# Kernel tuning notes

Measured on AMD Instinct MI355X. Metric: run time of the kernel, lower is better.

## Reference

```python
import jax, jax.numpy as jnp
import numpy as np
import math

D_MODEL = 1024
NUM_HEADS = 16
NUM_LAYERS = 4
D_FF = 4096
TEXT_DIM = 512
B, SV, ST = 4, 2048, 100
EPS = 1e-5


def positional_encoding(seq_len, d):
    pos = jnp.arange(seq_len, dtype=jnp.float32)[:, None]
    div = jnp.exp(jnp.arange(0, d, 2, dtype=jnp.float32) * (-math.log(10000.0) / d))
    pe = jnp.zeros((seq_len, d), dtype=jnp.float32)
    pe = pe.at[:, 0::2].set(jnp.sin(pos * div))
    pe = pe.at[:, 1::2].set(jnp.cos(pos * div))
    return pe  # [seq_len, d]


def layer_norm(x, g, b):
    mu = jnp.mean(x, axis=-1, keepdims=True)
    var = jnp.mean(jnp.square(x - mu), axis=-1, keepdims=True)
    return (x - mu) * jax.lax.rsqrt(var + EPS) * g + b


def setup_inputs() -> dict:
    key = jax.random.key(0)
    ks = jax.random.split(key, 24)
    s = 0.02
    inp = {
        "video": jax.random.normal(ks[0], (B, SV, D_MODEL), jnp.float32),
        "text": jax.random.normal(ks[1], (B, ST, TEXT_DIM), jnp.float32),
        "text_mask": jnp.ones((B, ST), jnp.int32),
        # stacked per-layer params, weights stored [in, out]
        "Wq_w": jax.random.normal(ks[2], (NUM_LAYERS, D_MODEL, D_MODEL)) * s,
        "Wq_b": jnp.zeros((NUM_LAYERS, D_MODEL)),
        "Wk_w": jax.random.normal(ks[3], (NUM_LAYERS, TEXT_DIM, D_MODEL)) * s,
        "Wk_b": jnp.zeros((NUM_LAYERS, D_MODEL)),
        "Wv_w": jax.random.normal(ks[4], (NUM_LAYERS, TEXT_DIM, D_MODEL)) * s,
        "Wv_b": jnp.zeros((NUM_LAYERS, D_MODEL)),
        "Wo_w": jax.random.normal(ks[5], (NUM_LAYERS, D_MODEL, D_MODEL)) * s,
        "Wo_b": jnp.zeros((NUM_LAYERS, D_MODEL)),
        "fc1_w": jax.random.normal(ks[6], (NUM_LAYERS, D_MODEL, D_FF)) * s,
        "fc1_b": jnp.zeros((NUM_LAYERS, D_FF)),
        "fc2_w": jax.random.normal(ks[7], (NUM_LAYERS, D_FF, D_MODEL)) * s,
        "fc2_b": jnp.zeros((NUM_LAYERS, D_MODEL)),
        "n2_g": jnp.ones((NUM_LAYERS, D_MODEL)),
        "n2_b": jnp.zeros((NUM_LAYERS, D_MODEL)),
        "n3_g": jnp.ones((NUM_LAYERS, D_MODEL)),
        "n3_b": jnp.zeros((NUM_LAYERS, D_MODEL)),
    }
    return inp


def cross_attn_layer(video, text, mask, wq, bq, wk, bk, wv, bv, wo, bo):
    Bv, Sq, D = video.shape
    H, dk = NUM_HEADS, D_MODEL // NUM_HEADS
    q = (video @ wq + bq).reshape(Bv, Sq, H, dk).transpose(0, 2, 1, 3)  # bhqd
    k = (text @ wk + bk).reshape(Bv, -1, H, dk).transpose(0, 2, 1, 3)   # bhkd
    v = (text @ wv + bv).reshape(Bv, -1, H, dk).transpose(0, 2, 1, 3)
    scores = jnp.einsum("bhqd,bhkd->bhqk", q, k) / math.sqrt(dk)
    scores = jnp.where(mask, scores, jnp.float32(-1e9))
    probs = jax.nn.softmax(scores, axis=-1)
    out = jnp.einsum("bhqk,bhkd->bhqd", probs, v)
    out = out.transpose(0, 2, 1, 3).reshape(Bv, Sq, D)
    return out @ wo + bo


def reference(video, text, text_mask, Wq_w, Wq_b, Wk_w, Wk_b, Wv_w, Wv_b,
              Wo_w, Wo_b, fc1_w, fc1_b, fc2_w, fc2_b, n2_g, n2_b, n3_g, n3_b):
    video = video + positional_encoding(SV, D_MODEL)[None, :video.shape[1]]
    text = text + positional_encoding(ST, TEXT_DIM)[None, :text.shape[1]]
    mask = (text_mask != 0)[:, None, None, :]  # [B,1,1,St]
    for l in range(NUM_LAYERS):
        attn = cross_attn_layer(video, text, mask,
                                Wq_w[l], Wq_b[l], Wk_w[l], Wk_b[l],
                                Wv_w[l], Wv_b[l], Wo_w[l], Wo_b[l])
        video = layer_norm(video + attn, n2_g[l], n2_b[l])
        ff = jax.nn.relu(video @ fc1_w[l] + fc1_b[l]) @ fc2_w[l] + fc2_b[l]
        video = layer_norm(video + ff, n3_g[l], n3_b[l])
    return video
```

## Files before the change

kernel.cpp:

```cpp
#include <hip/hip_runtime.h>
#include <cstdint>
#include <cstddef>

typedef unsigned short u16;
typedef __attribute__((ext_vector_type(8))) __bf16 bf16x8;
typedef __attribute__((ext_vector_type(4))) float f32x4;

__device__ __forceinline__ f32x4 mfma_16x16x32(bf16x8 a, bf16x8 b, f32x4 c) {
  return __builtin_amdgcn_mfma_f32_16x16x32_bf16(a, b, c, 0, 0, 0);
}

__device__ __forceinline__ u16 f2bf(float f) {
  union { float f; uint32_t u; } c; c.f = f;
  uint32_t u = c.u + 0x7FFFu + ((c.u >> 16) & 1u);
  return (u16)(u >> 16);
}

__device__ __forceinline__ float bf2f(u16 x) {
  union { uint32_t u; float f; } c; c.u = ((uint32_t)x) << 16;
  return c.f;
}

__device__ __forceinline__ void gload_lds16(const void* g, void* l) {
  __builtin_amdgcn_global_load_lds(
      (__attribute__((address_space(1))) void*)(uintptr_t)g,
      (__attribute__((address_space(3))) void*)l, 16, 0, 0);
}

template<int MR, bool OUT_BF16, bool RELU, bool ACC>
__global__ __launch_bounds__(512, 2) void gemm_ring(
    const u16* __restrict__ A, int lda, const u16* __restrict__ Bt, int ldb,
    const float* __restrict__ bias, void* Cout, int ldc,
    int M, int N, int K)
{
  constexpr int BM = MR * 32;
  constexpr int SLOT = (BM + 256) * 32;
  __shared__ u16 ring[4 * SLOT];

  const int tid = threadIdx.x;
  const int lane = tid & 63, wave = tid >> 6;
  const int wm = wave >> 2, wn = wave & 3;
  const int m0 = blockIdx.x * BM, n0 = blockIdx.y * 256;

  const int cA0 = tid;
  const int rA0 = cA0 >> 2;
  const u16* gA0 = A + (size_t)(m0 + rA0) * lda + (((cA0 & 3) ^ (rA0 & 3)) * 8);
  const int cA1 = tid + 512;
  const int rA1 = cA1 >> 2;
  const u16* gA1 = A + (size_t)(m0 + (MR == 8 ? rA1 : 0)) * lda + (((cA1 & 3) ^ (rA1 & 3)) * 8);
  const int cB0 = tid, cB1 = tid + 512;
  const int rB0 = cB0 >> 2, rB1 = cB1 >> 2;
  const u16* gB0 = Bt + (size_t)(n0 + rB0) * ldb + (((cB0 & 3) ^ (rB0 & 3)) * 8);
  const u16* gB1 = Bt + (size_t)(n0 + rB1) * ldb + (((cB1 & 3) ^ (rB1 & 3)) * 8);

  const int NK = K >> 5;

  auto STAGE = [&](int s) {
    u16* Sb = &ring[(s & 3) * SLOT];
    const int ko = s * 32;
    gload_lds16(gA0 + ko, Sb + cA0 * 8);
    if constexpr (MR == 8) gload_lds16(gA1 + ko, Sb + cA1 * 8);
    gload_lds16(gB0 + ko, Sb + BM * 32 + cB0 * 8);
    gload_lds16(gB1 + ko, Sb + BM * 32 + cB1 * 8);
  };
  auto WAITV = [&](int ahead) {
    if (ahead >= 2) {
      if constexpr (MR == 8) asm volatile("s_waitcnt vmcnt(8)" ::: "memory");
      else                   asm volatile("s_waitcnt vmcnt(6)" ::: "memory");
    } else if (ahead == 1) {
      if constexpr (MR == 8) asm volatile("s_waitcnt vmcnt(4)" ::: "memory");
      else                   asm volatile("s_waitcnt vmcnt(3)" ::: "memory");
    } else {
      asm volatile("s_waitcnt vmcnt(0)" ::: "memory");
    }
    __builtin_amdgcn_sched_barrier(0);
  };

  const int fr = lane & 15, g = lane >> 4;
  const int sw = g ^ (fr & 3);
  const int foff = fr * 32 + sw * 8;

  f32x4 acc[MR][4];
  #pragma unroll
  for (int m = 0; m < MR; m++)
    #pragma unroll
    for (int n = 0; n < 4; n++) acc[m][n] = f32x4{0.f, 0.f, 0.f, 0.f};

  for (int i = 0; i < 3; ++i) if (i < NK) STAGE(i);
  {
    int im = (NK - 1 < 2) ? NK - 1 : 2;
    WAITV(im);
  }
  __builtin_amdgcn_s_barrier();
  __builtin_amdgcn_sched_barrier(0);

  for (int s = 0; s < NK; ++s) {
    const u16* Sb = &ring[(s & 3) * SLOT];
    const u16* As = Sb;
    const u16* Bs = Sb + BM * 32;

    bf16x8 bf[4];
    #pragma unroll
    for (int n = 0; n < 4; n++)
      bf[n] = *(const bf16x8*)(Bs + (wn * 64 + n * 16) * 32 + foff);
    {
      bf16x8 af[MR / 2];
      #pragma unroll
      for (int m = 0; m < MR / 2; m++)
        af[m] = *(const bf16x8*)(As + (wm * (MR * 16) + m * 16) * 32 + foff);
      if (s + 3 < NK) STAGE(s + 3);
      __builtin_amdgcn_s_barrier();
      asm volatile("s_waitcnt lgkmcnt(0)" ::: "memory");
      __builtin_amdgcn_sched_barrier(0);
      __builtin_amdgcn_s_setprio(1);
      #pragma unroll
      for (int m = 0; m < MR / 2; m++)
        #pragma unroll
        for (int n = 0; n < 4; n++)
          acc[m][n] = mfma_16x16x32(af[m], bf[n], acc[m][n]);
      __builtin_amdgcn_s_setprio(0);
      __builtin_amdgcn_s_barrier();
      __builtin_amdgcn_sched_barrier(0);
    }
    {
      bf16x8 af[MR / 2];
      #pragma unroll
      for (int m = 0; m < MR / 2; m++)
        af[m] = *(const bf16x8*)(As + (wm * (MR * 16) + (m + MR / 2) * 16) * 32 + foff);
      __builtin_amdgcn_s_barrier();
      asm volatile("s_waitcnt lgkmcnt(0)" ::: "memory");
      __builtin_amdgcn_sched_barrier(0);
      __builtin_amdgcn_s_setprio(1);
      #pragma unroll
      for (int m = 0; m < MR / 2; m++)
        #pragma unroll
        for (int n = 0; n < 4; n++)
          acc[m + MR / 2][n] = mfma_16x16x32(af[m], bf[n], acc[m + MR / 2][n]);
      __builtin_amdgcn_s_setprio(0);
      {
        int im = (s + 3 < NK - 1) ? s + 3 : NK - 1;
        WAITV(im - (s + 1));
      }
      __builtin_amdgcn_s_barrier();
      __builtin_amdgcn_sched_barrier(0);
    }
  }

  #pragma unroll
  for (int n = 0; n < 4; n++) {
    const int gcol = n0 + wn * 64 + n * 16 + fr;
    const float bv = bias ? bias[gcol] : 0.f;
    #pragma unroll
    for (int m = 0; m < MR; m++) {
      #pragma unroll
      for (int r = 0; r < 4; r++) {
        const int grow = m0 + wm * (MR * 16) + m * 16 + g * 4 + r;
        float v = acc[m][n][r] + bv;
        if (ACC) v += bf2f(((const u16*)Cout)[(size_t)grow * ldc + gcol]);
        if (RELU) v = fmaxf(v, 0.f);
        if (OUT_BF16) ((u16*)Cout)[(size_t)grow * ldc + gcol] = f2bf(v);
        else         ((float*)Cout)[(size_t)grow * ldc + gcol] = v;
      }
    }
  }
}

template<bool TRANS>
__global__ __launch_bounds__(256, 2) void gemm_bt(
    const u16* __restrict__ A, int lda, const u16* __restrict__ Bt, int ldb,
    const float* __restrict__ bias, u16* Cout, int ldc,
    int M, int N, int K)
{
  __shared__ u16 ldsA[128 * 32];
  __shared__ u16 ldsB[128 * 32];

  const int tid = threadIdx.x;
  const int lane = tid & 63, wave = tid >> 6;
  const int wr = wave >> 1, wc = wave & 1;
  const int m0 = blockIdx.x * 128, n0 = blockIdx.y * 128;

  const int c0 = tid, c1 = tid + 256;
  const int ar0 = c0 >> 2, ak0 = (c0 & 3) * 8;
  const int ar1 = c1 >> 2, ak1 = (c1 & 3) * 8;

  const bool av0 = (m0 + ar0) < M;
  const bool av1 = (m0 + ar1) < M;
  const u16* Ag0 = A + (size_t)(m0 + ar0) * lda + ak0;
  const u16* Ag1 = A + (size_t)(m0 + ar1) * lda + ak1;
  const u16* Bg0 = Bt + (size_t)(n0 + ar0) * ldb + ak0;
  const u16* Bg1 = Bt + (size_t)(n0 + ar1) * ldb + ak1;

  f32x4 acc[4][4] = {};
  const int fr = lane & 15, fo = (lane >> 4) * 8;

  for (int k0 = 0; k0 < K; k0 += 32) {
    if (av0) gload_lds16(Ag0 + k0, &ldsA[c0 * 8]);
    if (av1) gload_lds16(Ag1 + k0, &ldsA[c1 * 8]);
    gload_lds16(Bg0 + k0, &ldsB[c0 * 8]);
    gload_lds16(Bg1 + k0, &ldsB[c1 * 8]);
    asm volatile("s_waitcnt vmcnt(0)" ::: "memory");
    __syncthreads();

    bf16x8 af[4], bfr[4];
    #pragma unroll
    for (int m = 0; m < 4; m++)
      af[m] = *(const bf16x8*)&ldsA[(wr * 64 + m * 16 + fr) * 32 + fo];
    #pragma unroll
    for (int n = 0; n < 4; n++)
      bfr[n] = *(const bf16x8*)&ldsB[(wc * 64 + n * 16 + fr) * 32 + fo];
    #pragma unroll
    for (int m = 0; m < 4; m++)
      #pragma unroll
      for (int n = 0; n < 4; n++)
        acc[m][n] = mfma_16x16x32(af[m], bfr[n], acc[m][n]);
    __syncthreads();
  }

  const int g = lane >> 4;
  #pragma unroll
  for (int m = 0; m < 4; m++) {
    #pragma unroll
    for (int n = 0; n < 4; n++) {
      const int gcol = n0 + wc * 64 + n * 16 + fr;
      const float bv = bias[gcol];
      #pragma unroll
      for (int r = 0; r < 4; r++) {
        const int grow = m0 + wr * 64 + m * 16 + g * 4 + r;
        if (grow < M) {
          float v = acc[m][n][r] + bv;
          if (TRANS) {
            int bb = grow / 100, jj = grow - bb * 100;
            int h = gcol >> 6, d = gcol & 63;
            Cout[(size_t)(((bb * 16 + h) * 64 + d)) * 128 + jj] = f2bf(v);
          } else {
            Cout[(size_t)grow * ldc + gcol] = f2bf(v);
          }
        }
      }
    }
  }
}

__global__ void wconv_t(const float* __restrict__ src, u16* __restrict__ dst,
                        int K, int N)
{
  __shared__ float tile[32][33];
  const int n0 = blockIdx.x * 32, k0 = blockIdx.y * 32;
  const int tx = threadIdx.x, ty = threadIdx.y;
  #pragma unroll
  for (int i = 0; i < 4; i++)
    tile[ty + i * 8][tx] = src[(size_t)(k0 + ty + i * 8) * N + n0 + tx];
  __syncthreads();
  #pragma unroll
  for (int i = 0; i < 4; i++)
    dst[(size_t)(n0 + ty + i * 8) * K + k0 + tx] = f2bf(tile[tx][ty + i * 8]);
}

__global__ __launch_bounds__(256) void pe_video_k(const float* __restrict__ video,
                                                  u16* __restrict__ vbf)
{
  const int r = blockIdx.x;
  const int s = r & 2047;
  const int d0 = threadIdx.x * 4;
  const size_t base = (size_t)r * 1024 + d0;
  float4 v = *(const float4*)&video[base];
  const float coef = -9.210340371976184f / 1024.f;
  float o[4];
  float in[4] = {v.x, v.y, v.z, v.w};
  #pragma unroll
  for (int i = 0; i < 4; i++) {
    int d = d0 + i;
    int j = d >> 1;
    float dv = expf((float)(2 * j) * coef);
    float arg = (float)s * dv;
    float pe = (d & 1) ? cosf(arg) : sinf(arg);
    o[i] = in[i] + pe;
  }
  uint2 pk;
  pk.x = (uint32_t)f2bf(o[0]) | ((uint32_t)f2bf(o[1]) << 16);
  pk.y = (uint32_t)f2bf(o[2]) | ((uint32_t)f2bf(o[3]) << 16);
  *(uint2*)&vbf[base] = pk;
}

__global__ __launch_bounds__(128) void pe_text_k(const float* __restrict__ text,
                                                 u16* __restrict__ tbf)
{
  const int r = blockIdx.x;
  const int s = r % 100;
  const int d0 = threadIdx.x * 4;
  const size_t base = (size_t)r * 512 + d0;
  float4 v = *(const float4*)&text[base];
  const float coef = -9.210340371976184f / 512.f;
  float o[4];
  float in[4] = {v.x, v.y, v.z, v.w};
  #pragma unroll
  for (int i = 0; i < 4; i++) {
    int d = d0 + i;
    int j = d >> 1;
    float dv = expf((float)(2 * j) * coef);
    float arg = (float)s * dv;
    float pe = (d & 1) ? cosf(arg) : sinf(arg);
    o[i] = in[i] + pe;
  }
  uint2 pk;
  pk.x = (uint32_t)f2bf(o[0]) | ((uint32_t)f2bf(o[1]) << 16);
  pk.y = (uint32_t)f2bf(o[2]) | ((uint32_t)f2bf(o[3]) << 16);
  *(uint2*)&tbf[base] = pk;
}

template<bool LAST>
__global__ __launch_bounds__(256) void ln2(const u16* __restrict__ xin,
                                           const u16* __restrict__ delta,
                                           const float* __restrict__ gamma,
                                           const float* __restrict__ beta,
                                           u16* __restrict__ xbf,
                                           float* __restrict__ fout)
{
  const int row = blockIdx.x;
  const size_t base = (size_t)row * 1024;
  const int t = threadIdx.x;
  const int d0 = t * 4;
  uint2 xv = *(const uint2*)&xin[base + d0];
  uint2 dv = *(const uint2*)&delta[base + d0];
  float v0 = bf2f((u16)(xv.x & 0xFFFF)) + bf2f((u16)(dv.x & 0xFFFF));
  float v1 = bf2f((u16)(xv.x >> 16))    + bf2f((u16)(dv.x >> 16));
  float v2 = bf2f((u16)(xv.y & 0xFFFF)) + bf2f((u16)(dv.y & 0xFFFF));
  float v3 = bf2f((u16)(xv.y >> 16))    + bf2f((u16)(dv.y >> 16));
  float s = v0 + v1 + v2 + v3;
  float q = v0 * v0 + v1 * v1 + v2 * v2 + v3 * v3;
  #pragma unroll
  for (int d = 32; d >= 1; d >>= 1) { s += __shfl_xor(s, d); q += __shfl_xor(q, d); }
  __shared__ float red[8];
  const int lane = t & 63, w = t >> 6;
  if (lane == 0) { red[w] = s; red[4 + w] = q; }
  __syncthreads();
  float S = red[0] + red[1] + red[2] + red[3];
  float Qs = red[4] + red[5] + red[6] + red[7];
  const float mu = S * (1.f / 1024.f);
  const float var = Qs * (1.f / 1024.f) - mu * mu;
  const float rs = rsqrtf(var + 1e-5f);
  float4 gv = *(const float4*)&gamma[d0];
  float4 bv = *(const float4*)&beta[d0];
  float o0 = (v0 - mu) * rs * gv.x + bv.x;
  float o1 = (v1 - mu) * rs * gv.y + bv.y;
  float o2 = (v2 - mu) * rs * gv.z + bv.z;
  float o3 = (v3 - mu) * rs * gv.w + bv.w;
  if (LAST) {
    *(float4*)&fout[base + d0] = make_float4(o0, o1, o2, o3);
  } else {
    uint2 pk;
    pk.x = (uint32_t)f2bf(o0) | ((uint32_t)f2bf(o1) << 16);
    pk.y = (uint32_t)f2bf(o2) | ((uint32_t)f2bf(o3) << 16);
    *(uint2*)&xbf[base + d0] = pk;
  }
}

__global__ __launch_bounds__(256) void attn_v2(
    const u16* __restrict__ Q, const u16* __restrict__ Kb,
    const u16* __restrict__ Vtb, const int* __restrict__ mask,
    u16* __restrict__ Out)
{
  __shared__ u16 ldsP[64 * 136];

  const int tid = threadIdx.x, lane = tid & 63, w = tid >> 6;
  const int qb = blockIdx.x, bh = blockIdx.y;
  const int b = bh >> 4, h = bh & 15;
  const int fr = lane & 15, g = lane >> 4, fo = g * 8;

  const size_t qrow = (size_t)(b * 2048 + qb * 64 + w * 16 + fr) * 1024 + h * 64;
  bf16x8 qf0 = *(const bf16x8*)&Q[qrow + fo];
  bf16x8 qf1 = *(const bf16x8*)&Q[qrow + 32 + fo];

  float madd[7];
  #pragma unroll
  for (int t = 0; t < 7; t++) {
    int col = t * 16 + fr;
    int mv = (col < 100) ? mask[b * 100 + col] : 0;
    madd[t] = mv ? 0.f : -1e30f;
  }

  float sc[7][4];
  #pragma unroll
  for (int t = 0; t < 7; t++) {
    int col = t * 16 + fr;
    int jr = (col < 100) ? col : 99;
    const u16* kp = Kb + (size_t)(b * 100 + jr) * 1024 + h * 64;
    bf16x8 kf0 = *(const bf16x8*)&kp[fo];
    bf16x8 kf1 = *(const bf16x8*)&kp[32 + fo];
    f32x4 a = {};
    a = mfma_16x16x32(qf0, kf0, a);
    a = mfma_16x16x32(qf1, kf1, a);
    #pragma unroll
    for (int r = 0; r < 4; r++)
      sc[t][r] = a[r] * 0.125f + madd[t];
  }

  #pragma unroll
  for (int r = 0; r < 4; r++) {
    float m = sc[0][r];
    #pragma unroll
    for (int t = 1; t < 7; t++) m = fmaxf(m, sc[t][r]);
    #pragma unroll
    for (int d = 8; d >= 1; d >>= 1) m = fmaxf(m, __shfl_xor(m, d));
    float ssum = 0.f;
    #pragma unroll
    for (int t = 0; t < 7; t++) { float p = __expf(sc[t][r] - m); sc[t][r] = p; ssum += p; }
    #pragma unroll
    for (int d = 8; d >= 1; d >>= 1) ssum += __shfl_xor(ssum, d);
    float is = 1.f / ssum;
    #pragma unroll
    for (int t = 0; t < 7; t++)
      ldsP[(w * 16 + g * 4 + r) * 136 + t * 16 + fr] = f2bf(sc[t][r] * is);
  }
  {
    u16* zp = &ldsP[(w * 16 + fr) * 136 + 112 + g * 6];
    #pragma unroll
    for (int i = 0; i < 6; i++) zp[i] = 0;
  }

  bf16x8 pa[4];
  #pragma unroll
  for (int kk = 0; kk < 4; kk++)
    pa[kk] = *(const bf16x8*)&ldsP[(w * 16 + fr) * 136 + kk * 32 + fo];
  const u16* vtbase = Vtb + (size_t)bh * 64 * 128;
  #pragma unroll
  for (int nt = 0; nt < 4; nt++) {
    f32x4 a = {};
    #pragma unroll
    for (int kk = 0; kk < 4; kk++) {
      bf16x8 vf = *(const bf16x8*)&vtbase[(size_t)(nt * 16 + fr) * 128 + kk * 32 + fo];
      a = mfma_16x16x32(pa[kk], vf, a);
    }
    #pragma unroll
    for (int r = 0; r < 4; r++) {
      size_t orow = (size_t)(b * 2048 + qb * 64 + w * 16 + g * 4 + r) * 1024 + h * 64 + nt * 16 + fr;
      Out[orow] = f2bf(a[r]);
    }
  }
}

extern "C" void kernel_launch(void* const* d_in, const int* in_sizes, int n_in,
                              void* d_out, int out_size, void* d_ws, size_t ws_size,
                              hipStream_t stream) {
  const float* video = (const float*)d_in[0];
  const float* text  = (const float*)d_in[1];
  const int*   text_mask = (const int*)d_in[2];
  const float* Wq_w = (const float*)d_in[3];
  const float* Wq_b = (const float*)d_in[4];
  const float* Wk_w = (const float*)d_in[5];
  const float* Wk_b = (const float*)d_in[6];
  const float* Wv_w = (const float*)d_in[7];
  const float* Wv_b = (const float*)d_in[8];
  const float* Wo_w = (const float*)d_in[9];
  const float* Wo_b = (const float*)d_in[10];
  const float* fc1_w = (const float*)d_in[11];
  const float* fc1_b = (const float*)d_in[12];
  const float* fc2_w = (const float*)d_in[13];
  const float* fc2_b = (const float*)d_in[14];
  const float* n2_g = (const float*)d_in[15];
  const float* n2_b = (const float*)d_in[16];
  const float* n3_g = (const float*)d_in[17];
  const float* n3_b = (const float*)d_in[18];

  char* ws = (char*)d_ws;
  size_t off = 0;
  auto alloc = [&](size_t bytes) {
    char* p = ws + off;
    off += (bytes + 255) & ~(size_t)255;
    return p;
  };
  u16* vbf = (u16*)alloc((size_t)8192 * 1024 * 2);
  u16* tbf = (u16*)alloc((size_t)400 * 512 * 2);
  u16* wqT = (u16*)alloc((size_t)1024 * 1024 * 2);
  u16* wkT = (u16*)alloc((size_t)1024 * 512 * 2);
  u16* wvT = (u16*)alloc((size_t)1024 * 512 * 2);
  u16* woT = (u16*)alloc((size_t)1024 * 1024 * 2);
  u16* f1T = (u16*)alloc((size_t)4096 * 1024 * 2);
  u16* f2T = (u16*)alloc((size_t)1024 * 4096 * 2);
  char* S = alloc((size_t)35192832);
  u16* qbf  = (u16*)S;
  u16* kbf  = (u16*)(S + 16777216);
  u16* abf  = (u16*)(S + 16777216 + 1638400);
  u16* h1c  = (u16*)S;
  u16* vtb  = (u16*)alloc((size_t)64 * 64 * 128 * 2);
  u16* dbf  = (u16*)alloc((size_t)8192 * 1024 * 2);
  float* fout = (float*)d_out;

  hipMemsetAsync(vtb, 0, (size_t)64 * 64 * 128 * 2, stream);

  pe_video_k<<<8192, 256, 0, stream>>>(video, vbf);
  pe_text_k<<<400, 128, 0, stream>>>(text, tbf);

  dim3 tb(32, 8, 1);
  for (int l = 0; l < 4; ++l) {
    wconv_t<<<dim3(32, 32), tb, 0, stream>>>(Wq_w + (size_t)l * 1024 * 1024, wqT, 1024, 1024);
    wconv_t<<<dim3(32, 16), tb, 0, stream>>>(Wk_w + (size_t)l * 512 * 1024, wkT, 512, 1024);
    wconv_t<<<dim3(32, 16), tb, 0, stream>>>(Wv_w + (size_t)l * 512 * 1024, wvT, 512, 1024);
    wconv_t<<<dim3(32, 32), tb, 0, stream>>>(Wo_w + (size_t)l * 1024 * 1024, woT, 1024, 1024);
    wconv_t<<<dim3(128, 32), tb, 0, stream>>>(fc1_w + (size_t)l * 1024 * 4096, f1T, 1024, 4096);
    wconv_t<<<dim3(32, 128), tb, 0, stream>>>(fc2_w + (size_t)l * 4096 * 1024, f2T, 4096, 1024);

    gemm_ring<4, true, false, false><<<dim3(64, 4), 512, 0, stream>>>(
        vbf, 1024, wqT, 1024, Wq_b + l * 1024, qbf, 1024, 8192, 1024, 1024);
    gemm_bt<false><<<dim3(4, 8), 256, 0, stream>>>(
        tbf, 512, wkT, 512, Wk_b + l * 1024, kbf, 1024, 400, 1024, 512);
    gemm_bt<true><<<dim3(4, 8), 256, 0, stream>>>(
        tbf, 512, wvT, 512, Wv_b + l * 1024, vtb, 1024, 400, 1024, 512);
    attn_v2<<<dim3(32, 64), 256, 0, stream>>>(qbf, kbf, vtb, text_mask, abf);
    gemm_ring<4, true, false, false><<<dim3(64, 4), 512, 0, stream>>>(
        abf, 1024, woT, 1024, Wo_b + l * 1024, dbf, 1024, 8192, 1024, 1024);
    ln2<false><<<8192, 256, 0, stream>>>(vbf, dbf, n2_g + l * 1024, n2_b + l * 1024, vbf, nullptr);

    for (int c = 0; c < 2; ++c) {
      gemm_ring<8, true, true, false><<<dim3(32, 8), 512, 0, stream>>>(
          vbf, 1024, f1T + (size_t)c * 2048 * 1024, 1024,
          fc1_b + l * 4096 + c * 2048, h1c, 2048, 8192, 2048, 1024);
      if (c == 0)
        gemm_ring<4, true, false, false><<<dim3(64, 4), 512, 0, stream>>>(
            h1c, 2048, f2T + (size_t)c * 2048, 4096,
            fc2_b + l * 1024, dbf, 1024, 8192, 1024, 2048);
      else
        gemm_ring<4, true, false, true><<<dim3(64, 4), 512, 0, stream>>>(
            h1c, 2048, f2T + (size_t)c * 2048, 4096,
            nullptr, dbf, 1024, 8192, 1024, 2048);
    }
    if (l == 3)
      ln2<true><<<8192, 256, 0, stream>>>(vbf, dbf, n3_g + l * 1024, n3_b + l * 1024, nullptr, fout);
    else
      ln2<false><<<8192, 256, 0, stream>>>(vbf, dbf, n3_g + l * 1024, n3_b + l * 1024, vbf, nullptr);
  }
}
```

Before: 1.395 ms.

## Cut GEMM main loop to one barrier per k-step and change LDS swizzle

```diff
diff --git a/kernel.cpp b/kernel.cpp
--- a/kernel.cpp
+++ b/kernel.cpp
@@ -42,16 +42,14 @@
   const int wm = wave >> 2, wn = wave & 3;
   const int m0 = blockIdx.x * BM, n0 = blockIdx.y * 256;
 
-  const int cA0 = tid;
-  const int rA0 = cA0 >> 2;
-  const u16* gA0 = A + (size_t)(m0 + rA0) * lda + (((cA0 & 3) ^ (rA0 & 3)) * 8);
-  const int cA1 = tid + 512;
-  const int rA1 = cA1 >> 2;
-  const u16* gA1 = A + (size_t)(m0 + (MR == 8 ? rA1 : 0)) * lda + (((cA1 & 3) ^ (rA1 & 3)) * 8);
-  const int cB0 = tid, cB1 = tid + 512;
-  const int rB0 = cB0 >> 2, rB1 = cB1 >> 2;
-  const u16* gB0 = Bt + (size_t)(n0 + rB0) * ldb + (((cB0 & 3) ^ (rB0 & 3)) * 8);
-  const u16* gB1 = Bt + (size_t)(n0 + rB1) * ldb + (((cB1 & 3) ^ (rB1 & 3)) * 8);
+  const int cA0 = tid, rA0 = cA0 >> 2;
+  const u16* gA0 = A + (size_t)(m0 + rA0) * lda + (((cA0 & 3) ^ ((rA0 >> 1) & 3)) * 8);
+  const int cA1 = tid + 512, rA1 = cA1 >> 2;
+  const u16* gA1 = A + (size_t)(m0 + (MR == 8 ? rA1 : 0)) * lda + (((cA1 & 3) ^ ((rA1 >> 1) & 3)) * 8);
+  const int cB0 = tid, rB0 = cB0 >> 2;
+  const int cB1 = tid + 512, rB1 = cB1 >> 2;
+  const u16* gB0 = Bt + (size_t)(n0 + rB0) * ldb + (((cB0 & 3) ^ ((rB0 >> 1) & 3)) * 8);
+  const u16* gB1 = Bt + (size_t)(n0 + rB1) * ldb + (((cB1 & 3) ^ ((rB1 >> 1) & 3)) * 8);
 
   const int NK = K >> 5;
 
@@ -73,12 +71,10 @@
     } else {
       asm volatile("s_waitcnt vmcnt(0)" ::: "memory");
     }
-    __builtin_amdgcn_sched_barrier(0);
   };
 
   const int fr = lane & 15, g = lane >> 4;
-  const int sw = g ^ (fr & 3);
-  const int foff = fr * 32 + sw * 8;
+  const int foff = fr * 32 + ((g ^ ((fr >> 1) & 3)) * 8);
 
   f32x4 acc[MR][4];
   #pragma unroll
@@ -86,64 +82,56 @@
     #pragma unroll
     for (int n = 0; n < 4; n++) acc[m][n] = f32x4{0.f, 0.f, 0.f, 0.f};
 
-  for (int i = 0; i < 3; ++i) if (i < NK) STAGE(i);
-  {
-    int im = (NK - 1 < 2) ? NK - 1 : 2;
-    WAITV(im);
-  }
+  for (int i = 0; i < 3 && i < NK; ++i) STAGE(i);
+  WAITV(NK - 1 < 2 ? NK - 1 : 2);
   __builtin_amdgcn_s_barrier();
   __builtin_amdgcn_sched_barrier(0);
 
   for (int s = 0; s < NK; ++s) {
-    const u16* Sb = &ring[(s & 3) * SLOT];
-    const u16* As = Sb;
-    const u16* Bs = Sb + BM * 32;
+    const u16* As = &ring[(s & 3) * SLOT];
+    const u16* Bs = As + BM * 32;
 
     bf16x8 bf[4];
     #pragma unroll
     for (int n = 0; n < 4; n++)
       bf[n] = *(const bf16x8*)(Bs + (wn * 64 + n * 16) * 32 + foff);
-    {
-      bf16x8 af[MR / 2];
+    bf16x8 af[4];
+    #pragma unroll
+    for (int m = 0; m < 4; m++)
+      af[m] = *(const bf16x8*)(As + (wm * (MR * 16) + m * 16) * 32 + foff);
+
+    if (s + 3 < NK) STAGE(s + 3);
+
+    __builtin_amdgcn_s_setprio(1);
+    #pragma unroll
+    for (int m = 0; m < 4; m++)
       #pragma unroll
-      for (int m = 0; m < MR / 2; m++)
-        af[m] = *(const bf16x8*)(As + (wm * (MR * 16) + m * 16) * 32 + foff);
-      if (s + 3 < NK) STAGE(s + 3);
-      __builtin_amdgcn_s_barrier();
-      asm volatile("s_waitcnt lgkmcnt(0)" ::: "memory");
-      __builtin_amdgcn_sched_barrier(0);
+      for (int n = 0; n < 4; n++)
+        acc[m][n] = mfma_16x16x32(af[m], bf[n], acc[m][n]);
+    __builtin_amdgcn_s_setprio(0);
+
+    if constexpr (MR == 8) {
+      bf16x8 af2[4];
+      #pragma unroll
+      for (int m = 0; m < 4; m++)
+        af2[m] = *(const bf16x8*)(As + (wm * 128 + (m + 4) * 16) * 32 + foff);
       __builtin_amdgcn_s_setprio(1);
       #pragma unroll
-      for (int m = 0; m < MR / 2; m++)
+      for (int m = 0; m < 4; m++)
         #pragma unroll
         for (int n = 0; n < 4; n++)
-          acc[m][n] = mfma_16x16x32(af[m], bf[n], acc[m][n]);
+          acc[m + 4][n] = mfma_16x16x32(af2[m], bf[n], acc[m + 4][n]);
       __builtin_amdgcn_s_setprio(0);
-      __builtin_amdgcn_s_barrier();
-      __builtin_amdgcn_sched_barrier(0);
-    }
+    }
+
     {
-      bf16x8 af[MR / 2];
-      #pragma unroll
-      for (int m = 0; m < MR / 2; m++)
-        af[m] = *(const bf16x8*)(As + (wm * (MR * 16) + (m + MR / 2) * 16) * 32 + foff);
-      __builtin_amdgcn_s_barrier();
-      asm volatile("s_waitcnt lgkmcnt(0)" ::: "memory");
-      __builtin_amdgcn_sched_barrier(0);
-      __builtin_amdgcn_s_setprio(1);
-      #pragma unroll
-      for (int m = 0; m < MR / 2; m++)
-        #pragma unroll
-        for (int n = 0; n < 4; n++)
-          acc[m + MR / 2][n] = mfma_16x16x32(af[m], bf[n], acc[m + MR / 2][n]);
-      __builtin_amdgcn_s_setprio(0);
-      {
-        int im = (s + 3 < NK - 1) ? s + 3 : NK - 1;
-        WAITV(im - (s + 1));
-      }
-      __builtin_amdgcn_s_barrier();
-      __builtin_amdgcn_sched_barrier(0);
-    }
+      int im = (s + 3 < NK - 1) ? s + 3 : NK - 1;
+      WAITV(im - (s + 1));
+    }
+    asm volatile("s_waitcnt lgkmcnt(0)" ::: "memory");
+    __builtin_amdgcn_sched_barrier(0);
+    __builtin_amdgcn_s_barrier();
+    __builtin_amdgcn_sched_barrier(0);
   }
 
   #pragma unroll
```

New measurement: 1.314 ms. 5.8% less time.
